# Kernel tuning notes

Measured on AMD Instinct MI355X. Metric: run time of the kernel, lower is better.

## Reference

```python
import jax, jax.numpy as jnp
import numpy as np

# distilled LLaVA-style decoder: nf4-quantized linears + LoRA(q/k/v/o) + gumbel-softmax -> embedding einsum
B, S, D, H, L = 1, 2048, 2048, 16, 2
DH = D // H
DFF, V, R, BLK = 8192, 32000, 8, 64
LORA_SCALE = 16.0 / R  # alpha / r
TAU = 1.0
SQRT_DH = float(np.sqrt(DH))

# bitsandbytes NF4 codebook (16 values)
NF4 = jnp.array([-1.0, -0.6961928009986877, -0.5250730514526367, -0.39491748809814453,
                 -0.28444138169288635, -0.18477343022823334, -0.09105003625154495, 0.0,
                 0.07958029955625534, 0.16093020141124725, 0.24611230194568634,
                 0.33791524171829224, 0.44070982933044434, 0.5626170039176941,
                 0.7229568362236023, 1.0], dtype=jnp.float32)


def dequant(idx, scale):
    # idx [..., out, in] int in [0,16); scale [..., out, in//BLK] per-block absmax
    return NF4[idx] * jnp.repeat(scale, BLK, axis=-1)


def rmsnorm(x, w):
    return x * jax.lax.rsqrt(jnp.mean(x * x, axis=-1, keepdims=True) + 1e-6) * w


def setup_inputs():
    key = jax.random.key(0)
    k = jax.random.split(key, 12)
    return {
        "input_ids": jax.random.randint(k[0], (B, S), 0, V, dtype=jnp.int32),
        "u": jax.random.uniform(k[1], (B, S, V), dtype=jnp.float32),
        "emb": jax.random.normal(k[2], (V, D), dtype=jnp.float32) * 0.02,
        "attn_scale": jax.random.uniform(k[3], (L, 4, D, D // BLK), minval=0.005, maxval=0.02, dtype=jnp.float32),
        "ffn_gu_scale": jax.random.uniform(k[4], (L, 2, DFF, D // BLK), minval=0.005, maxval=0.02, dtype=jnp.float32),
        "ffn_d_scale": jax.random.uniform(k[5], (L, D, DFF // BLK), minval=0.005, maxval=0.02, dtype=jnp.float32),
        "lora_A": jax.random.normal(k[6], (L, 4, R, D), dtype=jnp.float32) * 0.01,
        "lora_B": jax.random.normal(k[7], (L, 4, D, R), dtype=jnp.float32) * 0.01,
        "norm_w": jnp.ones((L, 2, D), dtype=jnp.float32),
        "final_norm_w": jnp.ones((D,), dtype=jnp.float32),
        "attn_idx": jax.random.randint(k[8], (L, 4, D, D), 0, 16, dtype=jnp.int32),
        "ffn_gu_idx": jax.random.randint(k[9], (L, 2, DFF, D), 0, 16, dtype=jnp.int32),
        "ffn_d_idx": jax.random.randint(k[10], (L, D, DFF), 0, 16, dtype=jnp.int32),
    }


def reference(input_ids, u, emb, attn_scale, ffn_gu_scale, ffn_d_scale,
              lora_A, lora_B, norm_w, final_norm_w, attn_idx, ffn_gu_idx, ffn_d_idx):
    h = emb[input_ids]  # [B, S, D]
    causal = jnp.tril(jnp.ones((S, S), dtype=bool))
    for l in range(L):
        x = rmsnorm(h, norm_w[l, 0])
        w = dequant(attn_idx[l], attn_scale[l])  # [4, D, D] dequantized q/k/v/o weights

        def proj(i, t):
            # nf4 linear + LoRA adapter (y = t W^T + (t A^T) B^T * alpha/r)
            return t @ w[i].T + ((t @ lora_A[l, i].T) @ lora_B[l, i].T) * LORA_SCALE

        q = proj(0, x).reshape(B, S, H, DH)
        k_ = proj(1, x).reshape(B, S, H, DH)
        v = proj(2, x).reshape(B, S, H, DH)
        scores = jnp.einsum('bqhd,bkhd->bhqk', q, k_) / SQRT_DH
        scores = jnp.where(causal, scores, -1e30)
        p = jax.nn.softmax(scores, axis=-1)
        o = jnp.einsum('bhqk,bkhd->bqhd', p, v).reshape(B, S, D)
        h = h + proj(3, o)

        x = rmsnorm(h, norm_w[l, 1])
        wgu = dequant(ffn_gu_idx[l], ffn_gu_scale[l])  # [2, DFF, D] gate/up
        wd = dequant(ffn_d_idx[l], ffn_d_scale[l])     # [D, DFF] down
        h = h + (jax.nn.silu(x @ wgu[0].T) * (x @ wgu[1].T)) @ wd.T

    h = rmsnorm(h, final_norm_w)
    logits = h @ emb.T  # [B, S, V]
    # gumbel_softmax(tau, hard=False): softmax((logits + G)/tau), G = -log(-log(U))
    gnoise = -jnp.log(-jnp.log(u + 1e-10) + 1e-10)
    g = jax.nn.softmax((logits + gnoise) / TAU, axis=-1)
    soft_embeddings = jnp.einsum('bsv,vd->bsd', g, emb)
    return soft_embeddings, logits
```

## Files before the change

kernel.cpp:

```cpp
#include <hip/hip_runtime.h>
#include <hip/hip_bf16.h>

typedef unsigned short u16;
typedef unsigned int u32;
typedef __bf16 bf16t;
typedef bf16t bf16x8 __attribute__((ext_vector_type(8)));
typedef float f32x4 __attribute__((ext_vector_type(4)));

constexpr int S_   = 2048;
constexpr int D_   = 2048;
constexpr int H_   = 16;
constexpr int DH_  = 128;
constexpr int L_   = 2;
constexpr int DFF_ = 8192;
constexpr int V_   = 32000;
constexpr int R_   = 8;

#define MFMA16(a, b, c) __builtin_amdgcn_mfma_f32_16x16x32_bf16(a, b, c, 0, 0, 0)

__constant__ float c_nf4[16] = {
  -1.0f, -0.6961928009986877f, -0.5250730514526367f, -0.39491748809814453f,
  -0.28444138169288635f, -0.18477343022823334f, -0.09105003625154495f, 0.0f,
  0.07958029955625534f, 0.16093020141124725f, 0.24611230194568634f,
  0.33791524171829224f, 0.44070982933044434f, 0.5626170039176941f,
  0.7229568362236023f, 1.0f };

__device__ __forceinline__ u16 f2bf(float f) {
  union { float f; u32 u; } v; v.f = f;
  u32 r = v.u + 0x7fffu + ((v.u >> 16) & 1u);
  return (u16)(r >> 16);
}
__device__ __forceinline__ float bf2f(u16 h) {
  union { u32 u; float f; } v; v.u = ((u32)h) << 16; return v.f;
}

__global__ __launch_bounds__(256) void k_gather(const int* __restrict__ ids,
                                                const float* __restrict__ emb,
                                                float* __restrict__ h) {
  int t = blockIdx.x * 256 + threadIdx.x;
  int s = t >> 11;
  int d = t & 2047;
  h[t] = emb[(size_t)ids[s] * D_ + d];
}

__global__ __launch_bounds__(256) void k_rmsnorm(const float* __restrict__ in,
                                                 const float* __restrict__ w,
                                                 u16* __restrict__ out) {
  int s = blockIdx.x;
  const float* x = in + (size_t)s * D_;
  float ss = 0.f;
  for (int d = threadIdx.x; d < D_; d += 256) { float v = x[d]; ss += v * v; }
#pragma unroll
  for (int m = 1; m < 64; m <<= 1) ss += __shfl_xor(ss, m, 64);
  __shared__ float sh[4];
  if ((threadIdx.x & 63) == 0) sh[threadIdx.x >> 6] = ss;
  __syncthreads();
  ss = sh[0] + sh[1] + sh[2] + sh[3];
  float sc = rsqrtf(ss * (1.0f / D_) + 1e-6f);
  u16* o = out + (size_t)s * D_;
  for (int d = threadIdx.x; d < D_; d += 256) o[d] = f2bf(x[d] * sc * w[d]);
}

__global__ __launch_bounds__(256) void k_dequant(const int* __restrict__ idx,
                                                 const float* __restrict__ scale,
                                                 u16* __restrict__ out, int kshift) {
  size_t t = (size_t)blockIdx.x * 256 + threadIdx.x;
  size_t e = t * 8;
  int k = (int)(e & ((1u << kshift) - 1));
  size_t n = e >> kshift;
  float s = scale[(n << (kshift - 6)) + (k >> 6)];
  int4 i0 = *(const int4*)(idx + e);
  int4 i1 = *(const int4*)(idx + e + 4);
  uint4 o;
  o.x = (u32)f2bf(c_nf4[i0.x] * s) | ((u32)f2bf(c_nf4[i0.y] * s) << 16);
  o.y = (u32)f2bf(c_nf4[i0.z] * s) | ((u32)f2bf(c_nf4[i0.w] * s) << 16);
  o.z = (u32)f2bf(c_nf4[i1.x] * s) | ((u32)f2bf(c_nf4[i1.y] * s) << 16);
  o.w = (u32)f2bf(c_nf4[i1.z] * s) | ((u32)f2bf(c_nf4[i1.w] * s) << 16);
  *(uint4*)(out + e) = o;
}

__global__ __launch_bounds__(256) void k_f2b(const float* __restrict__ src,
                                             u16* __restrict__ dst) {
  size_t e = ((size_t)blockIdx.x * 256 + threadIdx.x) * 8;
  float4 f0 = *(const float4*)(src + e);
  float4 f1 = *(const float4*)(src + e + 4);
  uint4 o;
  o.x = (u32)f2bf(f0.x) | ((u32)f2bf(f0.y) << 16);
  o.y = (u32)f2bf(f0.z) | ((u32)f2bf(f0.w) << 16);
  o.z = (u32)f2bf(f1.x) | ((u32)f2bf(f1.y) << 16);
  o.w = (u32)f2bf(f1.z) | ((u32)f2bf(f1.w) << 16);
  *(uint4*)(dst + e) = o;
}

__global__ __launch_bounds__(256) void k_transpose(const float* __restrict__ src,
                                                   u16* __restrict__ dst) {
  __shared__ u16 tile[64][65];
  int v0 = blockIdx.x * 64, d0 = blockIdx.y * 64;
  int tid = threadIdx.x;
  int rr = tid >> 4, cc = (tid & 15) * 4;
#pragma unroll
  for (int j = 0; j < 4; ++j) {
    int r = j * 16 + rr;
    float4 f = *(const float4*)(src + (size_t)(v0 + r) * D_ + d0 + cc);
    tile[r][cc + 0] = f2bf(f.x); tile[r][cc + 1] = f2bf(f.y);
    tile[r][cc + 2] = f2bf(f.z); tile[r][cc + 3] = f2bf(f.w);
  }
  __syncthreads();
#pragma unroll
  for (int j = 0; j < 4; ++j) {
    int r = j * 16 + rr;
    ushort4 w;
    w.x = tile[cc + 0][r]; w.y = tile[cc + 1][r];
    w.z = tile[cc + 2][r]; w.w = tile[cc + 3][r];
    *(ushort4*)(dst + (size_t)(d0 + r) * V_ + v0 + cc) = w;
  }
}

enum { OUT_F32 = 0, OUT_F32_ACC = 1, OUT_BF16 = 2 };

template<int OUTMODE>
__global__ __launch_bounds__(512, 2) void k_gemm256(const u16* __restrict__ A, int lda,
                                                    const u16* __restrict__ B, int ldb,
                                                    void* __restrict__ Cv, int ldc,
                                                    int Kc, size_t zstride) {
  __shared__ u16 As[2][256][64];
  __shared__ u16 Bs[2][256][64];
  const int tid = threadIdx.x;
  const int lane = tid & 63, w = tid >> 6;
  const int wr = w >> 2, wc = w & 3;
  const int g = (lane >> 4), l15 = lane & 15, sl7 = lane & 7;

  const int nbx = gridDim.x;
  const int cpx = (nbx * gridDim.y) >> 3;
  int lin = blockIdx.y * nbx + blockIdx.x;
  int swz = (lin & 7) * cpx + (lin >> 3);
  const int m0 = (swz / nbx) * 256;
  const int n0 = (swz % nbx) * 256;

  A += (size_t)blockIdx.z * Kc;
  B += (size_t)blockIdx.z * Kc;
  float* Cf = (float*)Cv + (size_t)blockIdx.z * zstride;

  const int NT = Kc >> 6;
  const int srow = w * 8 + (lane >> 3);
  const int sch  = (lane & 7) ^ (lane >> 3);

  auto stageA = [&](int half, int tile) {
    const u16* src = A + (size_t)(m0 + half * 128 + srow) * lda + tile * 64 + sch * 8;
    u16* dst = &As[tile & 1][half * 128 + w * 8][0];
#pragma unroll
    for (int rnd = 0; rnd < 2; ++rnd)
      __builtin_amdgcn_global_load_lds(
          (const __attribute__((address_space(1))) void*)(src + (size_t)rnd * 64 * lda),
          (__attribute__((address_space(3))) void*)(dst + rnd * 64 * 64), 16, 0, 0);
  };
  auto stageB = [&](int half, int tile) {
    const u16* src = B + (size_t)(n0 + half * 128 + srow) * ldb + tile * 64 + sch * 8;
    u16* dst = &Bs[tile & 1][half * 128 + w * 8][0];
#pragma unroll
    for (int rnd = 0; rnd < 2; ++rnd)
      __builtin_amdgcn_global_load_lds(
          (const __attribute__((address_space(1))) void*)(src + (size_t)rnd * 64 * ldb),
          (__attribute__((address_space(3))) void*)(dst + rnd * 64 * 64), 16, 0, 0);
  };

  f32x4 acc[8][4] = {};
  bf16x8 areg[4][2], breg[2][2][2];

  stageB(0, 0); stageA(0, 0); stageB(1, 0); stageA(1, 0);
  if (NT > 1) {
    stageB(0, 1); stageA(0, 1);
    asm volatile("s_waitcnt vmcnt(4)" ::: "memory");
  } else {
    asm volatile("s_waitcnt vmcnt(0)" ::: "memory");
  }
  __builtin_amdgcn_s_barrier();

#define LOADA(QR)                                                                   \
  _Pragma("unroll") for (int m = 0; m < 4; ++m)                                     \
    _Pragma("unroll") for (int kh = 0; kh < 2; ++kh) {                              \
      int hr = wr * 128 + (QR) * 64 + m * 16 + l15;                                 \
      areg[m][kh] = *(const bf16x8*)(abase + hr * 64 + ((((kh << 2) | g) ^ sl7) << 3)); \
    }
#define LOADB(QC)                                                                   \
  _Pragma("unroll") for (int n = 0; n < 2; ++n)                                     \
    _Pragma("unroll") for (int kh = 0; kh < 2; ++kh) {                              \
      int br = wc * 64 + (QC) * 32 + n * 16 + l15;                                  \
      breg[QC][n][kh] = *(const bf16x8*)(bbase + br * 64 + ((((kh << 2) | g) ^ sl7) << 3)); \
    }
#define QPHASE(QR, QC)                                                              \
  __builtin_amdgcn_s_setprio(1);                                                    \
  _Pragma("unroll") for (int m = 0; m < 4; ++m)                                     \
    _Pragma("unroll") for (int n = 0; n < 2; ++n)                                   \
      _Pragma("unroll") for (int kh = 0; kh < 2; ++kh)                              \
        acc[(QR) * 4 + m][(QC) * 2 + n] = __builtin_amdgcn_mfma_f32_16x16x32_bf16(  \
            areg[m][kh], breg[QC][n][kh], acc[(QR) * 4 + m][(QC) * 2 + n], 0, 0, 0); \
  __builtin_amdgcn_s_setprio(0);

  for (int t = 0; t < NT; ++t) {
    const u16* abase = &As[t & 1][0][0];
    const u16* bbase = &Bs[t & 1][0][0];
    LOADA(0); LOADB(0);
    if (t + 1 < NT) stageB(1, t + 1);
    QPHASE(0, 0);
    __builtin_amdgcn_s_barrier();
    LOADB(1);
    if (t + 1 < NT) stageA(1, t + 1);
    QPHASE(0, 1);
    __builtin_amdgcn_s_barrier();
    LOADA(1);
    if (t + 2 < NT) stageB(0, t + 2);
    QPHASE(1, 1);
    __builtin_amdgcn_s_barrier();
    if (t + 2 < NT) stageA(0, t + 2);
    QPHASE(1, 0);
    if (t + 1 < NT) {
      if (t + 1 == NT - 1) asm volatile("s_waitcnt vmcnt(0)" ::: "memory");
      else                 asm volatile("s_waitcnt vmcnt(4)" ::: "memory");
    }
    __builtin_amdgcn_s_barrier();
  }
#undef LOADA
#undef LOADB
#undef QPHASE

  const int er = g * 4;
#pragma unroll
  for (int i = 0; i < 8; ++i)
#pragma unroll
    for (int j = 0; j < 4; ++j)
#pragma unroll
      for (int r = 0; r < 4; ++r) {
        int row = m0 + wr * 128 + i * 16 + er + r;
        int col = n0 + wc * 64 + j * 16 + l15;
        if (OUTMODE == OUT_BF16) {
          ((u16*)Cv)[(size_t)row * ldc + col] = f2bf(acc[i][j][r]);
        } else if (OUTMODE == OUT_F32_ACC) {
          Cf[(size_t)row * ldc + col] += acc[i][j][r];
        } else {
          Cf[(size_t)row * ldc + col] = acc[i][j][r];
        }
      }
}

__global__ __launch_bounds__(256) void k_red(const float* __restrict__ P,
                                             float* __restrict__ dst, int accmode) {
  size_t i = ((size_t)blockIdx.x * 256 + threadIdx.x) * 4;
  const size_t n = (size_t)4 * 1024 * 1024;
  float4 a = *(const float4*)(P + i);
  float4 b = *(const float4*)(P + n + i);
  float4 c = *(const float4*)(P + 2 * n + i);
  float4 d = *(const float4*)(P + 3 * n + i);
  float4 r;
  r.x = (a.x + b.x) + (c.x + d.x);
  r.y = (a.y + b.y) + (c.y + d.y);
  r.z = (a.z + b.z) + (c.z + d.z);
  r.w = (a.w + b.w) + (c.w + d.w);
  if (accmode) {
    float4 o = *(const float4*)(dst + i);
    r.x += o.x; r.y += o.y; r.z += o.z; r.w += o.w;
  }
  *(float4*)(dst + i) = r;
}

__global__ __launch_bounds__(256) void k_lora_down(const u16* __restrict__ X,
                                                   const float* __restrict__ A,
                                                   float* __restrict__ T, int nproj) {
  int s = blockIdx.x;
  int lane = threadIdx.x & 63, wv = threadIdx.x >> 6;
  const u16* x = X + (size_t)s * D_;
  for (int p = wv; p < nproj * R_; p += 4) {
    const float* a = A + (size_t)p * D_;
    float sum = 0.f;
    for (int d = lane; d < D_; d += 64) sum += bf2f(x[d]) * a[d];
#pragma unroll
    for (int m = 1; m < 64; m <<= 1) sum += __shfl_xor(sum, m, 64);
    if (lane == 0) T[(size_t)s * (nproj * R_) + p] = sum;
  }
}

__global__ __launch_bounds__(256) void k_lora_up(float* __restrict__ Y, int ystride,
                                                 const float* __restrict__ T,
                                                 const float* __restrict__ Bm, int nproj) {
  int t = blockIdx.x * 256 + threadIdx.x;
  int d = t & (D_ - 1);
  int si = t >> 11;
  int i = si % nproj;
  int s = si / nproj;
  const float* tp = T + ((size_t)s * nproj + i) * R_;
  const float* bp = Bm + ((size_t)i * D_ + d) * R_;
  float acc = 0.f;
#pragma unroll
  for (int r = 0; r < R_; r++) acc += tp[r] * bp[r];
  Y[(size_t)s * ystride + (size_t)i * D_ + d] += 2.0f * acc;
}

__global__ __launch_bounds__(256) void k_lora_up_qkv(const float* __restrict__ qkv,
                                                     const float* __restrict__ T,
                                                     const float* __restrict__ Bm,
                                                     u16* __restrict__ qkvb) {
  size_t t = ((size_t)blockIdx.x * 256 + threadIdx.x) * 4;
  int c = (int)(t % 6144);
  int s = (int)(t / 6144);
  int i = c >> 11, d = c & 2047;
  const float* tp = T + ((size_t)s * 3 + i) * R_;
  float4 q = *(const float4*)(qkv + t);
  ushort4 o;
  float v[4] = {q.x, q.y, q.z, q.w};
#pragma unroll
  for (int j = 0; j < 4; ++j) {
    const float* bp = Bm + ((size_t)i * D_ + d + j) * R_;
    float acc = 0.f;
#pragma unroll
    for (int r = 0; r < R_; r++) acc += tp[r] * bp[r];
    v[j] += 2.0f * acc;
  }
  o.x = f2bf(v[0]); o.y = f2bf(v[1]); o.z = f2bf(v[2]); o.w = f2bf(v[3]);
  *(ushort4*)(qkvb + t) = o;
}

__global__ __launch_bounds__(256) void k_vtrans(const u16* __restrict__ qkvb,
                                                u16* __restrict__ Vt) {
  __shared__ u16 t[64][136];
  int s0 = blockIdx.x * 64, hh = blockIdx.y;
  int tid = threadIdx.x;
#pragma unroll
  for (int it = 0; it < 4; ++it) {
    int e = it * 2048 + tid * 8;
    int sr = e >> 7, sc = e & 127;
    *(uint4*)&t[sr][sc] =
        *(const uint4*)(qkvb + (size_t)(s0 + sr) * 6144 + 4096 + hh * 128 + sc);
  }
  __syncthreads();
#pragma unroll
  for (int it = 0; it < 4; ++it) {
    int q = it * 256 + tid;
    int dh = q >> 3, sc = (q & 7) * 8;
    u16 e0 = t[sc + 0][dh], e1 = t[sc + 1][dh], e2 = t[sc + 2][dh], e3 = t[sc + 3][dh];
    u16 e4 = t[sc + 4][dh], e5 = t[sc + 5][dh], e6 = t[sc + 6][dh], e7 = t[sc + 7][dh];
    uint4 o;
    o.x = (u32)e0 | ((u32)e1 << 16);
    o.y = (u32)e2 | ((u32)e3 << 16);
    o.z = (u32)e4 | ((u32)e5 << 16);
    o.w = (u32)e6 | ((u32)e7 << 16);
    *(uint4*)(Vt + ((size_t)hh * DH_ + dh) * S_ + s0 + sc) = o;
  }
}

__global__ __launch_bounds__(256) void k_attn2(const u16* __restrict__ qkvb,
                                               const u16* __restrict__ Vt,
                                               u16* __restrict__ out) {
  __shared__ u16 Ks[2][64 * 128];
  __shared__ u16 VTs[2][128 * 64];
  __shared__ u16 PT[4][64 * 16];
  const int tid = threadIdx.x;
  const int lane = tid & 63, w = tid >> 6;
  const int g = lane >> 4, l4 = lane & 15;
  const int p = blockIdx.x;
  const int hh = blockIdx.y;
  const int ld = 6144;
  const float rs = 0.08838834764831845f;
  const int qa0 = p * 64, qb0 = (31 - p) * 64;
  const int ntb = 32 - p;
  char* pt_w = (char*)&PT[w][0];

  const int qga = qa0 + w * 16 + l4;
  const int qgb = qb0 + w * 16 + l4;

  bf16x8 qfa[4], qfb[4];
#pragma unroll
  for (int kh = 0; kh < 4; ++kh) {
    qfa[kh] = *(const bf16x8*)(qkvb + (size_t)qga * ld + hh * DH_ + kh * 32 + g * 8);
    qfb[kh] = *(const bf16x8*)(qkvb + (size_t)qgb * ld + hh * DH_ + kh * 32 + g * 8);
  }

  float ma = -3.0e38f, la = 0.f, mb = -3.0e38f, lb = 0.f;
  f32x4 acc_a[8] = {}, acc_b[8] = {};
  bf16x8 pba[2], pbb[2];

  auto stage = [&](int buf, int kt) {
    const int kv0 = kt * 64;
#pragma unroll
    for (int i = 0; i < 4; ++i) {
      int rl = (w * 4 + i) * 4 + (lane >> 4);
      int cs = (lane & 15) ^ ((rl & 7) ^ (((rl >> 3) & 3) << 1));
      __builtin_amdgcn_global_load_lds(
          (const __attribute__((address_space(1))) void*)(
              qkvb + (size_t)(kv0 + rl) * ld + 2048 + hh * DH_ + cs * 8),
          (__attribute__((address_space(3))) void*)(&Ks[buf][(w * 4 + i) * 512]), 16, 0, 0);
    }
#pragma unroll
    for (int i = 0; i < 4; ++i) {
      int dh = (w * 4 + i) * 8 + (lane >> 3);
      int cs = (lane & 7) ^ (dh & 7);
      __builtin_amdgcn_global_load_lds(
          (const __attribute__((address_space(1))) void*)(
              Vt + ((size_t)hh * DH_ + dh) * S_ + kv0 + cs * 8),
          (__attribute__((address_space(3))) void*)(&VTs[buf][(w * 4 + i) * 512]), 16, 0, 0);
    }
  };

  auto softpb = [&](f32x4* sv, float& m, float& l, f32x4* acc, int qg, bool diag,
                    int kv0, bf16x8* pb) {
    float pv[16];
    float tmax = -3.0e38f;
#pragma unroll
    for (int kb = 0; kb < 4; ++kb)
#pragma unroll
      for (int r = 0; r < 4; ++r) {
        float s = sv[kb][r] * rs;
        if (diag) {
          int kglob = kv0 + kb * 16 + g * 4 + r;
          if (kglob > qg) s = -1.0e30f;
        }
        pv[kb * 4 + r] = s;
        tmax = fmaxf(tmax, s);
      }
    tmax = fmaxf(tmax, __shfl_xor(tmax, 16, 64));
    tmax = fmaxf(tmax, __shfl_xor(tmax, 32, 64));
    float mn = fmaxf(m, tmax);
    float corr = __expf(m - mn);
    m = mn;
    float ps = 0.f;
#pragma unroll
    for (int i = 0; i < 16; ++i) { pv[i] = __expf(pv[i] - mn); ps += pv[i]; }
    ps += __shfl_xor(ps, 16, 64);
    ps += __shfl_xor(ps, 32, 64);
    l = l * corr + ps;
#pragma unroll
    for (int f = 0; f < 8; ++f) {
      acc[f][0] *= corr; acc[f][1] *= corr; acc[f][2] *= corr; acc[f][3] *= corr;
    }
#pragma unroll
    for (int kb = 0; kb < 4; ++kb)
#pragma unroll
      for (int r = 0; r < 4; ++r) {
        int key = kb * 16 + g * 4 + r;
        int byte = (key * 32 + l4 * 2) ^ (((key >> 3) & 3) << 5);
        *(u16*)(pt_w + byte) = f2bf(pv[kb * 4 + r]);
      }
#pragma unroll
    for (int ks = 0; ks < 2; ++ks) {
      union { bf16x8 v; u16 s[8]; } ub;
#pragma unroll
      for (int j = 0; j < 8; ++j) {
        int key = ks * 32 + g * 8 + j;
        int byte = (key * 32 + l4 * 2) ^ (((key >> 3) & 3) << 5);
        ub.s[j] = *(const u16*)(pt_w + byte);
      }
      pb[ks] = ub.v;
    }
  };

  stage(0, 0);
  asm volatile("s_waitcnt vmcnt(0)" ::: "memory");
  __syncthreads();

  for (int kt = 0; kt < ntb; ++kt) {
    const int kv0 = kt * 64;
    const int buf = kt & 1;
    if (kt + 1 < ntb) stage(buf ^ 1, kt + 1);

    const char* kb_base = (const char*)&Ks[buf][0];
    const char* vb_base = (const char*)&VTs[buf][0];
    const bool doa = (kt <= p);

    f32x4 sa[4] = {}, sb[4] = {};
#pragma unroll
    for (int kb = 0; kb < 4; ++kb) {
#pragma unroll
      for (int kh = 0; kh < 4; ++kh) {
        int key = kb * 16 + l4;
        int ch = (kh * 4 + g) ^ ((key & 7) ^ (((key >> 3) & 3) << 1));
        bf16x8 af = *(const bf16x8*)(kb_base + key * 256 + ch * 16);
        if (doa) sa[kb] = MFMA16(af, qfa[kh], sa[kb]);
        sb[kb] = MFMA16(af, qfb[kh], sb[kb]);
      }
    }

    if (doa) softpb(sa, ma, la, acc_a, qga, kt == p, kv0, pba);
    softpb(sb, mb, lb, acc_b, qgb, kt == ntb - 1, kv0, pbb);

#pragma unroll
    for (int f = 0; f < 8; ++f) {
#pragma unroll
      for (int ks = 0; ks < 2; ++ks) {
        int dh = f * 16 + l4;
        int ch = (ks * 4 + g) ^ (dh & 7);
        bf16x8 va = *(const bf16x8*)(vb_base + dh * 128 + ch * 16);
        if (doa) acc_a[f] = MFMA16(va, pba[ks], acc_a[f]);
        acc_b[f] = MFMA16(va, pbb[ks], acc_b[f]);
      }
    }

    if (kt + 1 < ntb) {
      asm volatile("s_waitcnt vmcnt(0)" ::: "memory");
      __syncthreads();
    }
  }

  float inva = 1.f / la, invb = 1.f / lb;
  u16* opa = out + (size_t)qga * D_ + hh * DH_;
  u16* opb = out + (size_t)qgb * D_ + hh * DH_;
#pragma unroll
  for (int f = 0; f < 8; ++f)
#pragma unroll
    for (int r = 0; r < 4; ++r) {
      opa[f * 16 + g * 4 + r] = f2bf(acc_a[f][r] * inva);
      opb[f * 16 + g * 4 + r] = f2bf(acc_b[f][r] * invb);
    }
}

__global__ __launch_bounds__(256) void k_silumul(u16* __restrict__ gu) {
  size_t i = ((size_t)blockIdx.x * 256 + threadIdx.x) * 4;
  int s = (int)(i >> 13);
  int f = (int)(i & 8191);
  u16* gp = gu + (size_t)s * (2 * DFF_) + f;
  ushort4 gt = *(ushort4*)gp;
  ushort4 up = *(ushort4*)(gp + DFF_);
  float g0 = bf2f(gt.x), g1 = bf2f(gt.y), g2 = bf2f(gt.z), g3 = bf2f(gt.w);
  float u0 = bf2f(up.x), u1 = bf2f(up.y), u2 = bf2f(up.z), u3 = bf2f(up.w);
  ushort4 o;
  o.x = f2bf(g0 / (1.f + __expf(-g0)) * u0);
  o.y = f2bf(g1 / (1.f + __expf(-g1)) * u1);
  o.z = f2bf(g2 / (1.f + __expf(-g2)) * u2);
  o.w = f2bf(g3 / (1.f + __expf(-g3)) * u3);
  *(ushort4*)gp = o;
}

__global__ __launch_bounds__(256) void k_gumbel(const float* __restrict__ logits,
                                                const float* __restrict__ u,
                                                u16* __restrict__ g) {
  int s = blockIdx.x;
  const float* lp = logits + (size_t)s * V_;
  const float* up = u + (size_t)s * V_;
  float m = -3.0e38f, l = 0.f;
  for (int v = threadIdx.x; v < V_; v += 256) {
    float z = lp[v] - __logf(-__logf(up[v] + 1e-10f) + 1e-10f);
    float mn = fmaxf(m, z);
    l = l * __expf(m - mn) + __expf(z - mn);
    m = mn;
  }
#pragma unroll
  for (int msk = 1; msk < 64; msk <<= 1) {
    float m2 = __shfl_xor(m, msk, 64), l2 = __shfl_xor(l, msk, 64);
    float mn = fmaxf(m, m2);
    l = l * __expf(m - mn) + l2 * __expf(m2 - mn);
    m = mn;
  }
  __shared__ float shm[4], shl[4];
  if ((threadIdx.x & 63) == 0) { shm[threadIdx.x >> 6] = m; shl[threadIdx.x >> 6] = l; }
  __syncthreads();
  float M = fmaxf(fmaxf(shm[0], shm[1]), fmaxf(shm[2], shm[3]));
  float L = shl[0] * __expf(shm[0] - M) + shl[1] * __expf(shm[1] - M) +
            shl[2] * __expf(shm[2] - M) + shl[3] * __expf(shm[3] - M);
  float inv = 1.f / L;
  u16* gp = g + (size_t)s * V_;
  for (int v = threadIdx.x; v < V_; v += 256) {
    float z = lp[v] - __logf(-__logf(up[v] + 1e-10f) + 1e-10f);
    gp[v] = f2bf(__expf(z - M) * inv);
  }
}

extern "C" void kernel_launch(void* const* d_in, const int* in_sizes, int n_in,
                              void* d_out, int out_size, void* d_ws, size_t ws_size,
                              hipStream_t stream) {
  const int*   ids        = (const int*)d_in[0];
  const float* u          = (const float*)d_in[1];
  const float* emb        = (const float*)d_in[2];
  const float* attn_scale = (const float*)d_in[3];
  const float* gu_scale   = (const float*)d_in[4];
  const float* dn_scale   = (const float*)d_in[5];
  const float* lora_A     = (const float*)d_in[6];
  const float* lora_B     = (const float*)d_in[7];
  const float* norm_w     = (const float*)d_in[8];
  const float* fnorm_w    = (const float*)d_in[9];
  const int*   attn_idx   = (const int*)d_in[10];
  const int*   gu_idx     = (const int*)d_in[11];
  const int*   dn_idx     = (const int*)d_in[12];

  float* out_se = (float*)d_out;
  float* out_lg = (float*)d_out + (size_t)S_ * D_;

  char* W = (char*)d_ws;
  float* h    = (float*)(W);
  u16*   xb   = (u16*)(W + ((size_t)16 << 20));
  float* qkv  = (float*)(W + ((size_t)24 << 20));
  u16*   qkvb = (u16*)(W + ((size_t)72 << 20));
  u16*   Vtb  = (u16*)(W + ((size_t)96 << 20));
  u16*   ob   = (u16*)(W + ((size_t)104 << 20));
  u16*   gub  = (u16*)(W + ((size_t)112 << 20));
  u16*   wdq  = (u16*)(W + ((size_t)176 << 20));
  float* Tl   = (float*)(W + ((size_t)240 << 20));
  u16*   embb = (u16*)(W);
  u16*   gsm  = (u16*)(W + ((size_t)125 << 20));
  u16*   embT = (u16*)(W);
  u16*   xbh  = (u16*)d_out;
  float* Pk   = (float*)(W + ((size_t)250 << 20));
  const bool big = ws_size >= ((size_t)314 << 20);
  const size_t ZS = (size_t)4 * 1024 * 1024;

  dim3 b256(256), b512(512);

  k_gather<<<dim3(S_ * D_ / 256), b256, 0, stream>>>(ids, emb, h);

  for (int l = 0; l < L_; ++l) {
    const int*   aidx = attn_idx + (size_t)l * 4 * D_ * D_;
    const float* ascl = attn_scale + (size_t)l * 4 * D_ * (D_ / 64);
    const float* lA   = lora_A + (size_t)l * 4 * R_ * D_;
    const float* lB   = lora_B + (size_t)l * 4 * D_ * R_;

    k_rmsnorm<<<dim3(S_), b256, 0, stream>>>(h, norm_w + (size_t)l * 2 * D_, xb);
    k_dequant<<<dim3(4 * D_ * D_ / 8 / 256), b256, 0, stream>>>(aidx, ascl, wdq, 11);
    k_gemm256<OUT_F32><<<dim3(3 * D_ / 256, 8), b512, 0, stream>>>(
        xb, D_, wdq, D_, qkv, 3 * D_, D_, 0);
    k_lora_down<<<dim3(S_), b256, 0, stream>>>(xb, lA, Tl, 3);
    k_lora_up_qkv<<<dim3(S_ * 3 * D_ / 4 / 256), b256, 0, stream>>>(qkv, Tl, lB, qkvb);
    k_vtrans<<<dim3(S_ / 64, H_), b256, 0, stream>>>(qkvb, Vtb);
    k_attn2<<<dim3(16, H_), b256, 0, stream>>>(qkvb, Vtb, ob);
    k_gemm256<OUT_F32_ACC><<<dim3(D_ / 256, 8), b512, 0, stream>>>(
        ob, D_, wdq + (size_t)3 * D_ * D_, D_, h, D_, D_, 0);
    k_lora_down<<<dim3(S_), b256, 0, stream>>>(ob, lA + (size_t)3 * R_ * D_, Tl, 1);
    k_lora_up<<<dim3(S_ * D_ / 256), b256, 0, stream>>>(h, D_, Tl, lB + (size_t)3 * D_ * R_, 1);

    k_rmsnorm<<<dim3(S_), b256, 0, stream>>>(h, norm_w + (size_t)l * 2 * D_ + D_, xb);
    k_dequant<<<dim3(2 * DFF_ * D_ / 8 / 256), b256, 0, stream>>>(
        gu_idx + (size_t)l * 2 * DFF_ * D_, gu_scale + (size_t)l * 2 * DFF_ * (D_ / 64), wdq, 11);
    k_gemm256<OUT_BF16><<<dim3(2 * DFF_ / 256, 8), b512, 0, stream>>>(
        xb, D_, wdq, D_, gub, 2 * DFF_, D_, 0);
    k_silumul<<<dim3(S_ * DFF_ / 4 / 256), b256, 0, stream>>>(gub);
    k_dequant<<<dim3(D_ * DFF_ / 8 / 256), b256, 0, stream>>>(
        dn_idx + (size_t)l * D_ * DFF_, dn_scale + (size_t)l * D_ * (DFF_ / 64), wdq, 13);
    if (big) {
      k_gemm256<OUT_F32><<<dim3(D_ / 256, 8, 4), b512, 0, stream>>>(
          gub, 2 * DFF_, wdq, DFF_, Pk, D_, DFF_ / 4, ZS);
      k_red<<<dim3(4096), b256, 0, stream>>>(Pk, h, 1);
    } else {
      k_gemm256<OUT_F32_ACC><<<dim3(D_ / 256, 8), b512, 0, stream>>>(
          gub, 2 * DFF_, wdq, DFF_, h, D_, DFF_, 0);
    }
  }

  k_rmsnorm<<<dim3(S_), b256, 0, stream>>>(h, fnorm_w, xbh);
  k_f2b<<<dim3(V_ * D_ / 8 / 256), b256, 0, stream>>>(emb, embb);
  k_gemm256<OUT_F32><<<dim3(V_ / 256, 8), b512, 0, stream>>>(
      xbh, D_, embb, D_, out_lg, V_, D_, 0);
  k_gumbel<<<dim3(S_), b256, 0, stream>>>(out_lg, u, gsm);
  k_transpose<<<dim3(V_ / 64, D_ / 64), b256, 0, stream>>>(emb, embT);
  if (big) {
    k_gemm256<OUT_F32><<<dim3(D_ / 256, 8, 4), b512, 0, stream>>>(
        gsm, V_, embT, V_, Pk, D_, V_ / 4, ZS);
    k_red<<<dim3(4096), b256, 0, stream>>>(Pk, out_se, 0);
  } else {
    k_gemm256<OUT_F32><<<dim3(D_ / 256, 8), b512, 0, stream>>>(
        gsm, V_, embT, V_, out_se, D_, V_, 0);
  }
}
```

Measured before the change: 2.493 ms.

## Prefetch full tiles two steps ahead and remap block swizzle column-major

The GEMM mainloop now issues each K-tile's A and B global-to-LDS loads in full, two iterations ahead, instead of spreading half-tile loads across the four compute phases. Extra barriers and explicit lgkmcnt waits are added before each MFMA phase. The vmcnt thresholds change to match. The tile swizzle now walks M fastest within each column group, which changes which blocks share L2 data. The added barriers may cost more than the longer load latency hiding gains.

```diff
diff --git a/kernel.cpp b/kernel.cpp
--- a/kernel.cpp
+++ b/kernel.cpp
@@ -130,12 +130,12 @@
   const int wr = w >> 2, wc = w & 3;
   const int g = (lane >> 4), l15 = lane & 15, sl7 = lane & 7;
 
-  const int nbx = gridDim.x;
-  const int cpx = (nbx * gridDim.y) >> 3;
-  int lin = blockIdx.y * nbx + blockIdx.x;
-  int swz = (lin & 7) * cpx + (lin >> 3);
-  const int m0 = (swz / nbx) * 256;
-  const int n0 = (swz % nbx) * 256;
+  const int gx = gridDim.x, gy = gridDim.y;
+  const int cpx = (gx * gy) >> 3;
+  int d = blockIdx.y * gx + blockIdx.x;
+  int swz = (d & 7) * cpx + (d >> 3);
+  const int m0 = (swz % gy) * 256;
+  const int n0 = (swz / gy) * 256;
 
   A += (size_t)blockIdx.z * Kc;
   B += (size_t)blockIdx.z * Kc;
@@ -167,10 +167,10 @@
   f32x4 acc[8][4] = {};
   bf16x8 areg[4][2], breg[2][2][2];
 
-  stageB(0, 0); stageA(0, 0); stageB(1, 0); stageA(1, 0);
+  stageB(0, 0); stageB(1, 0); stageA(0, 0); stageA(1, 0);
   if (NT > 1) {
-    stageB(0, 1); stageA(0, 1);
-    asm volatile("s_waitcnt vmcnt(4)" ::: "memory");
+    stageB(0, 1); stageB(1, 1); stageA(0, 1); stageA(1, 1);
+    asm volatile("s_waitcnt vmcnt(8)" ::: "memory");
   } else {
     asm volatile("s_waitcnt vmcnt(0)" ::: "memory");
   }
@@ -201,22 +201,26 @@
     const u16* abase = &As[t & 1][0][0];
     const u16* bbase = &Bs[t & 1][0][0];
     LOADA(0); LOADB(0);
-    if (t + 1 < NT) stageB(1, t + 1);
+    __builtin_amdgcn_s_barrier();
+    asm volatile("s_waitcnt lgkmcnt(0)" ::: "memory");
     QPHASE(0, 0);
     __builtin_amdgcn_s_barrier();
     LOADB(1);
-    if (t + 1 < NT) stageA(1, t + 1);
+    __builtin_amdgcn_s_barrier();
+    asm volatile("s_waitcnt lgkmcnt(0)" ::: "memory");
     QPHASE(0, 1);
     __builtin_amdgcn_s_barrier();
     LOADA(1);
-    if (t + 2 < NT) stageB(0, t + 2);
+    if (t + 2 < NT) { stageB(0, t + 2); stageB(1, t + 2); }
+    __builtin_amdgcn_s_barrier();
+    asm volatile("s_waitcnt lgkmcnt(0)" ::: "memory");
     QPHASE(1, 1);
     __builtin_amdgcn_s_barrier();
-    if (t + 2 < NT) stageA(0, t + 2);
+    if (t + 2 < NT) { stageA(0, t + 2); stageA(1, t + 2); }
     QPHASE(1, 0);
     if (t + 1 < NT) {
-      if (t + 1 == NT - 1) asm volatile("s_waitcnt vmcnt(0)" ::: "memory");
-      else                 asm volatile("s_waitcnt vmcnt(4)" ::: "memory");
+      if (t + 2 < NT) asm volatile("s_waitcnt vmcnt(8)" ::: "memory");
+      else            asm volatile("s_waitcnt vmcnt(0)" ::: "memory");
     }
     __builtin_amdgcn_s_barrier();
   }
```

New measurement: 2.461 ms. Within noise of the previous version (-1.3%).
